# Optimization experiments

Measured on AMD Instinct MI355X. Metric: run time of the kernel, lower is better.

The kernel has to match this reference:

```python
import jax, jax.numpy as jnp
import numpy as np

NUM_HEADS = 8


def setup_inputs() -> dict:
    key = jax.random.key(0)
    k1, k2 = jax.random.split(key)
    B, N_NB, N_C, D = 4, 4, 1024, 512
    d_h = D // NUM_HEADS
    x = jax.random.normal(k1, (B, N_NB, N_C, D), dtype=jnp.float32)
    # GAT-style attention vector a = [a1 || a2], per (batch, neighborhood, head, complex)
    attn_w = jax.random.normal(k2, (B, N_NB, NUM_HEADS, N_C, 2 * d_h), dtype=jnp.float32)
    return {"x": x, "attn_w": attn_w}


def reference(x, attn_w):
    # x: [B, n_neighborhood, n_complexes, D]
    B, N_NB, N_C, D = x.shape
    H = NUM_HEADS
    d_h = D // H
    # split into heads: [B, N_NB, H, N_C, d_h]  (matches reshape + transpose(2,3))
    xh = x.reshape(B, N_NB, N_C, H, d_h).transpose(0, 1, 3, 2, 4)
    # GAT concat-attention: e[b,n,h,i,j] = a1[b,n,h,i] . x_i + a2[b,n,h,i] . x_j
    # (decomposition avoids materializing the [.., N_C, N_C, 2*d_h] concat tensor
    #  that the original builds via repeat / repeat_interleave / cat)
    a1 = attn_w[..., :d_h]   # [B, N_NB, H, N_C, d_h]
    a2 = attn_w[..., d_h:]   # [B, N_NB, H, N_C, d_h]
    e_self = jnp.sum(xh * a1, axis=-1)                    # [B, N_NB, H, N_C]
    e_pair = jnp.einsum('bnhik,bnhjk->bnhij', a2, xh)      # [B, N_NB, H, N_C, N_C]
    scores = e_self[..., None] + e_pair                    # [B, N_NB, H, N_C, N_C]
    attn = jax.nn.softmax(scores, axis=-1)
    # transpose(2,3): heads back next to complexes -> [B, N_NB, N_C, H, N_C]
    return jnp.swapaxes(attn, 2, 3)
```

## Files before the change

### kernel.cpp

```cpp
#include <hip/hip_runtime.h>
#include <hip/hip_fp16.h>


typedef _Float16 half8 __attribute__((ext_vector_type(8)));
typedef float floatx4 __attribute__((ext_vector_type(4)));

#define N_C 1024

__global__ __launch_bounds__(256) void prep_kernel(
    const float* __restrict__ x, _Float16* __restrict__ xh16)
{
  int t = blockIdx.x * 256 + threadIdx.x;
  int kk  = t & 7;
  int row = (t >> 3) & 1023;
  int bnh = t >> 13;
  int bn = bnh >> 3, h = bnh & 7;
  const float* src = x + ((size_t)(bn * N_C + row) * 512) + h * 64 + kk * 8;
  _Float16* dst = xh16 + ((size_t)(bnh * N_C + row) * 64) + ((kk ^ (row & 7)) * 8);
  const float4* s4 = (const float4*)src;
  float4 u = s4[0], v = s4[1];
  half8 hv;
  hv[0] = (_Float16)u.x; hv[1] = (_Float16)u.y;
  hv[2] = (_Float16)u.z; hv[3] = (_Float16)u.w;
  hv[4] = (_Float16)v.x; hv[5] = (_Float16)v.y;
  hv[6] = (_Float16)v.z; hv[7] = (_Float16)v.w;
  *(half8*)dst = hv;
}

__global__ __launch_bounds__(256) void attn_kernel(
    const _Float16* __restrict__ xh16, const float* __restrict__ aw,
    float* __restrict__ out)
{
  __shared__ __align__(16) _Float16 lds[2 * 128 * 64];
  __shared__ float redsum[4][16];

  const int bx  = (blockIdx.x & 7) * 1024 + (blockIdx.x >> 3);
  const int bnh = bx >> 6;
  const int it  = bx & 63;
  const int bn  = bnh >> 3, h = bnh & 7;
  const int tid = threadIdx.x;
  const int w    = tid >> 6;
  const int lane = tid & 63;
  const int l16  = lane & 15;
  const int lq   = lane >> 4;

  const float* a2p = aw + ((size_t)bnh * N_C + it * 16 + l16) * 128 + 64;
  float4 u0 = *(const float4*)(a2p + lq * 8);
  float4 u1 = *(const float4*)(a2p + lq * 8 + 4);
  float4 u2 = *(const float4*)(a2p + 32 + lq * 8);
  float4 u3 = *(const float4*)(a2p + 32 + lq * 8 + 4);
  const float L2E = 1.4426950408889634f;
  half8 afrag0, afrag1;
  afrag0[0] = (_Float16)(u0.x * L2E); afrag0[1] = (_Float16)(u0.y * L2E);
  afrag0[2] = (_Float16)(u0.z * L2E); afrag0[3] = (_Float16)(u0.w * L2E);
  afrag0[4] = (_Float16)(u1.x * L2E); afrag0[5] = (_Float16)(u1.y * L2E);
  afrag0[6] = (_Float16)(u1.z * L2E); afrag0[7] = (_Float16)(u1.w * L2E);
  afrag1[0] = (_Float16)(u2.x * L2E); afrag1[1] = (_Float16)(u2.y * L2E);
  afrag1[2] = (_Float16)(u2.z * L2E); afrag1[3] = (_Float16)(u2.w * L2E);
  afrag1[4] = (_Float16)(u3.x * L2E); afrag1[5] = (_Float16)(u3.y * L2E);
  afrag1[6] = (_Float16)(u3.z * L2E); afrag1[7] = (_Float16)(u3.w * L2E);

  floatx4 acc[16];
  #pragma unroll
  for (int i = 0; i < 16; ++i) acc[i] = floatx4{0.f, 0.f, 0.f, 0.f};
  float rs = 0.f;

  const char* xbase = (const char*)(xh16 + (size_t)bnh * (N_C * 64));
  char* ldsb = (char*)lds;

  #define STAGE(c, b)                                                          \
    _Pragma("unroll")                                                          \
    for (int q = 0; q < 4; ++q) {                                              \
      int seg = (w * 4 + q) * 1024;                                            \
      __builtin_amdgcn_global_load_lds(                                        \
          (const __attribute__((address_space(1))) unsigned int*)              \
              (xbase + (c) * 16384 + seg + lane * 16),                         \
          (__attribute__((address_space(3))) unsigned int*)                    \
              (ldsb + (b) * 16384 + seg),                                      \
          16, 0, 0);                                                           \
    }

  STAGE(0, 0)
  #pragma unroll
  for (int c = 0; c < 8; ++c) {
    const int b = c & 1;
    __syncthreads();
    if (c < 7) STAGE(c + 1, b ^ 1)
    #pragma unroll
    for (int f = 0; f < 2; ++f) {
      int rl = w * 32 + f * 16 + l16;
      const char* p = ldsb + b * 16384 + rl * 128;
      const half8 b0 = *(const half8*)(p + (((lq    ) ^ (rl & 7)) << 4));
      const half8 b1 = *(const half8*)(p + (((lq + 4) ^ (rl & 7)) << 4));
      floatx4 v = acc[c * 2 + f];
      v = __builtin_amdgcn_mfma_f32_16x16x32_f16(b0, afrag0, v, 0, 0, 0);
      v = __builtin_amdgcn_mfma_f32_16x16x32_f16(b1, afrag1, v, 0, 0, 0);
      #pragma unroll
      for (int ri = 0; ri < 4; ++ri) {
        float e = __builtin_amdgcn_exp2f(v[ri]);
        v[ri] = e;
        rs += e;
      }
      acc[c * 2 + f] = v;
    }
  }

  rs += __shfl_xor(rs, 16);
  rs += __shfl_xor(rs, 32);
  if (lane < 16) redsum[w][lane] = rs;
  __syncthreads();
  const float inv = 1.0f / (redsum[0][l16] + redsum[1][l16] +
                            redsum[2][l16] + redsum[3][l16]);

  float* tb = (float*)lds;
  const int W = w * 2048;
  float* orow = out + (((size_t)(bn * N_C + it * 16) * 8 + h) * N_C);
  #pragma unroll
  for (int p = 0; p < 2; ++p) {
    #pragma unroll
    for (int c4 = 0; c4 < 4; ++c4) {
      #pragma unroll
      for (int f = 0; f < 2; ++f) {
        floatx4 v = acc[(p * 4 + c4) * 2 + f] * inv;
        int jl = c4 * 32 + f * 16 + lq * 4;
        *(floatx4*)(tb + W + l16 * 128 + (jl ^ ((l16 & 7) << 2))) = v;
      }
    }
    #pragma unroll
    for (int t = 0; t < 8; ++t) {
      int il = 2 * t + (lane >> 5);
      int jl = (lane & 31) * 4;
      floatx4 v = *(const floatx4*)(tb + W + il * 128 + (jl ^ ((il & 7) << 2)));
      int j = p * 512 + (jl >> 5) * 128 + w * 32 + (jl & 31);
      __builtin_nontemporal_store(v, (floatx4*)(orow + (size_t)il * 8192 + j));
    }
    if (p == 0) __syncthreads();
  }
}

extern "C" void kernel_launch(void* const* d_in, const int* in_sizes, int n_in,
                              void* d_out, int out_size, void* d_ws, size_t ws_size,
                              hipStream_t stream) {
  const float* x  = (const float*)d_in[0];
  const float* aw = (const float*)d_in[1];
  float* out = (float*)d_out;

  _Float16* xh16 = (_Float16*)d_ws;

  prep_kernel<<<4096, 256, 0, stream>>>(x, xh16);
  attn_kernel<<<8192, 256, 0, stream>>>(xh16, aw, out);
}
```

Measured before the change: 125.3 us.

## Fuse fp32-to-fp16 conversion into attention kernel and drop prep kernel

Removes the separate prep kernel that converted x to a swizzled fp16 workspace. Each attention block now loads fp32 x rows directly into registers, converts them to fp16, and writes them into swizzled LDS, with the global load issued before the MFMA work and the LDS write after it so the two overlap. This saves one kernel launch and the workspace write and read-back. The cost is double the L2 read traffic per block (fp32 instead of fp16) and more register pressure from the staging registers. An epilogue __syncthreads is also dropped, since each wave only touches its own LDS region there.

```diff
diff --git a/kernel.cpp b/kernel.cpp
--- a/kernel.cpp
+++ b/kernel.cpp
@@ -7,28 +7,8 @@
 
 #define N_C 1024
 
-__global__ __launch_bounds__(256) void prep_kernel(
-    const float* __restrict__ x, _Float16* __restrict__ xh16)
-{
-  int t = blockIdx.x * 256 + threadIdx.x;
-  int kk  = t & 7;
-  int row = (t >> 3) & 1023;
-  int bnh = t >> 13;
-  int bn = bnh >> 3, h = bnh & 7;
-  const float* src = x + ((size_t)(bn * N_C + row) * 512) + h * 64 + kk * 8;
-  _Float16* dst = xh16 + ((size_t)(bnh * N_C + row) * 64) + ((kk ^ (row & 7)) * 8);
-  const float4* s4 = (const float4*)src;
-  float4 u = s4[0], v = s4[1];
-  half8 hv;
-  hv[0] = (_Float16)u.x; hv[1] = (_Float16)u.y;
-  hv[2] = (_Float16)u.z; hv[3] = (_Float16)u.w;
-  hv[4] = (_Float16)v.x; hv[5] = (_Float16)v.y;
-  hv[6] = (_Float16)v.z; hv[7] = (_Float16)v.w;
-  *(half8*)dst = hv;
-}
-
 __global__ __launch_bounds__(256) void attn_kernel(
-    const _Float16* __restrict__ xh16, const float* __restrict__ aw,
+    const float* __restrict__ x, const float* __restrict__ aw,
     float* __restrict__ out)
 {
   __shared__ __align__(16) _Float16 lds[2 * 128 * 64];
@@ -65,27 +45,38 @@
   for (int i = 0; i < 16; ++i) acc[i] = floatx4{0.f, 0.f, 0.f, 0.f};
   float rs = 0.f;
 
-  const char* xbase = (const char*)(xh16 + (size_t)bnh * (N_C * 64));
-  char* ldsb = (char*)lds;
+  const int sr  = tid >> 1;
+  const int shh = tid & 1;
+  const float* xsrc = x + (((size_t)bn * N_C + sr) * 512) + h * 64 + shh * 32;
+  _Float16* sdst0 = lds + sr * 64;
 
-  #define STAGE(c, b)                                                          \
+  float4 st[8];
+  #define SLOAD(c)                                                             \
     _Pragma("unroll")                                                          \
-    for (int q = 0; q < 4; ++q) {                                              \
-      int seg = (w * 4 + q) * 1024;                                            \
-      __builtin_amdgcn_global_load_lds(                                        \
-          (const __attribute__((address_space(1))) unsigned int*)              \
-              (xbase + (c) * 16384 + seg + lane * 16),                         \
-          (__attribute__((address_space(3))) unsigned int*)                    \
-              (ldsb + (b) * 16384 + seg),                                      \
-          16, 0, 0);                                                           \
+    for (int q = 0; q < 8; ++q)                                                \
+      st[q] = *(const float4*)(xsrc + (size_t)(c) * 65536 + q * 4);
+
+  #define SWRITE(b)                                                            \
+    _Pragma("unroll")                                                          \
+    for (int o = 0; o < 4; ++o) {                                              \
+      half8 hv;                                                                \
+      hv[0] = (_Float16)st[2*o].x;   hv[1] = (_Float16)st[2*o].y;              \
+      hv[2] = (_Float16)st[2*o].z;   hv[3] = (_Float16)st[2*o].w;              \
+      hv[4] = (_Float16)st[2*o+1].x; hv[5] = (_Float16)st[2*o+1].y;            \
+      hv[6] = (_Float16)st[2*o+1].z; hv[7] = (_Float16)st[2*o+1].w;            \
+      int kk = shh * 4 + o;                                                    \
+      *(half8*)(sdst0 + (b) * 8192 + (((kk) ^ (sr & 7)) * 8)) = hv;            \
     }
 
-  STAGE(0, 0)
+  const char* ldsb = (const char*)lds;
+
+  SLOAD(0)
+  SWRITE(0)
   #pragma unroll
   for (int c = 0; c < 8; ++c) {
     const int b = c & 1;
     __syncthreads();
-    if (c < 7) STAGE(c + 1, b ^ 1)
+    if (c < 7) SLOAD(c + 1)
     #pragma unroll
     for (int f = 0; f < 2; ++f) {
       int rl = w * 32 + f * 16 + l16;
@@ -103,6 +94,7 @@
       }
       acc[c * 2 + f] = v;
     }
+    if (c < 7) SWRITE(b ^ 1)
   }
 
   rs += __shfl_xor(rs, 16);
@@ -134,7 +126,6 @@
       int j = p * 512 + (jl >> 5) * 128 + w * 32 + (jl & 31);
       __builtin_nontemporal_store(v, (floatx4*)(orow + (size_t)il * 8192 + j));
     }
-    if (p == 0) __syncthreads();
   }
 }
 
@@ -145,8 +136,5 @@
   const float* aw = (const float*)d_in[1];
   float* out = (float*)d_out;
 
-  _Float16* xh16 = (_Float16*)d_ws;
-
-  prep_kernel<<<4096, 256, 0, stream>>>(x, xh16);
-  attn_kernel<<<8192, 256, 0, stream>>>(xh16, aw, out);
+  attn_kernel<<<8192, 256, 0, stream>>>(x, aw, out);
 }
```

New measurement: 268.1 us. +114.0%, slower.

## Single-buffer LDS staging to raise occupancy, narrow output stores, swizzle prep blocks

Applied to the files above, without the earlier changes.

Halves the attention kernel's LDS by dropping the double buffer, so each chunk is loaded then synced before compute, and adds a launch-bounds hint for 6 blocks per SIMD. The epilogue transpose is reworked into 4 smaller groups with 8-byte nontemporal stores to fit the smaller LDS tile. The prep kernel's block index is also remapped. The intent is more resident blocks to hide the heavily store-bound output traffic, at the cost of losing load/compute overlap and using narrower stores.

```diff
diff --git a/kernel.cpp b/kernel.cpp
--- a/kernel.cpp
+++ b/kernel.cpp
@@ -4,13 +4,15 @@
 
 typedef _Float16 half8 __attribute__((ext_vector_type(8)));
 typedef float floatx4 __attribute__((ext_vector_type(4)));
+typedef float floatx2 __attribute__((ext_vector_type(2)));
 
 #define N_C 1024
 
 __global__ __launch_bounds__(256) void prep_kernel(
     const float* __restrict__ x, _Float16* __restrict__ xh16)
 {
-  int t = blockIdx.x * 256 + threadIdx.x;
+  const int bx = (blockIdx.x & 7) * 512 + (blockIdx.x >> 3);
+  int t = bx * 256 + threadIdx.x;
   int kk  = t & 7;
   int row = (t >> 3) & 1023;
   int bnh = t >> 13;
@@ -27,11 +29,11 @@
   *(half8*)dst = hv;
 }
 
-__global__ __launch_bounds__(256) void attn_kernel(
+__global__ __launch_bounds__(256, 6) void attn_kernel(
     const _Float16* __restrict__ xh16, const float* __restrict__ aw,
     float* __restrict__ out)
 {
-  __shared__ __align__(16) _Float16 lds[2 * 128 * 64];
+  __shared__ __align__(16) _Float16 lds[128 * 64];
   __shared__ float redsum[4][16];
 
   const int bx  = (blockIdx.x & 7) * 1024 + (blockIdx.x >> 3);
@@ -68,28 +70,26 @@
   const char* xbase = (const char*)(xh16 + (size_t)bnh * (N_C * 64));
   char* ldsb = (char*)lds;
 
-  #define STAGE(c, b)                                                          \
+  #define STAGE(c)                                                             \
     _Pragma("unroll")                                                          \
     for (int q = 0; q < 4; ++q) {                                              \
       int seg = (w * 4 + q) * 1024;                                            \
       __builtin_amdgcn_global_load_lds(                                        \
           (const __attribute__((address_space(1))) unsigned int*)              \
               (xbase + (c) * 16384 + seg + lane * 16),                         \
-          (__attribute__((address_space(3))) unsigned int*)                    \
-              (ldsb + (b) * 16384 + seg),                                      \
+          (__attribute__((address_space(3))) unsigned int*)(ldsb + seg),       \
           16, 0, 0);                                                           \
     }
 
-  STAGE(0, 0)
   #pragma unroll
   for (int c = 0; c < 8; ++c) {
-    const int b = c & 1;
     __syncthreads();
-    if (c < 7) STAGE(c + 1, b ^ 1)
+    STAGE(c)
+    __syncthreads();
     #pragma unroll
     for (int f = 0; f < 2; ++f) {
       int rl = w * 32 + f * 16 + l16;
-      const char* p = ldsb + b * 16384 + rl * 128;
+      const char* p = ldsb + rl * 128;
       const half8 b0 = *(const half8*)(p + (((lq    ) ^ (rl & 7)) << 4));
       const half8 b1 = *(const half8*)(p + (((lq + 4) ^ (rl & 7)) << 4));
       floatx4 v = acc[c * 2 + f];
@@ -113,28 +113,27 @@
                             redsum[2][l16] + redsum[3][l16]);
 
   float* tb = (float*)lds;
-  const int W = w * 2048;
+  const int W = w * 1024;
   float* orow = out + (((size_t)(bn * N_C + it * 16) * 8 + h) * N_C);
   #pragma unroll
-  for (int p = 0; p < 2; ++p) {
+  for (int g = 0; g < 4; ++g) {
     #pragma unroll
-    for (int c4 = 0; c4 < 4; ++c4) {
+    for (int cc = 0; cc < 2; ++cc) {
       #pragma unroll
       for (int f = 0; f < 2; ++f) {
-        floatx4 v = acc[(p * 4 + c4) * 2 + f] * inv;
-        int jl = c4 * 32 + f * 16 + lq * 4;
-        *(floatx4*)(tb + W + l16 * 128 + (jl ^ ((l16 & 7) << 2))) = v;
+        floatx4 v = acc[(2 * g + cc) * 2 + f] * inv;
+        int jp = cc * 32 + f * 16 + lq * 4;
+        *(floatx4*)(tb + W + l16 * 64 + (jp ^ ((l16 & 7) << 2))) = v;
       }
     }
     #pragma unroll
     for (int t = 0; t < 8; ++t) {
-      int il = 2 * t + (lane >> 5);
-      int jl = (lane & 31) * 4;
-      floatx4 v = *(const floatx4*)(tb + W + il * 128 + (jl ^ ((il & 7) << 2)));
-      int j = p * 512 + (jl >> 5) * 128 + w * 32 + (jl & 31);
-      __builtin_nontemporal_store(v, (floatx4*)(orow + (size_t)il * 8192 + j));
+      int il  = 2 * t + (lane >> 5);
+      int jp2 = (lane & 31) * 2;
+      floatx2 v = *(const floatx2*)(tb + W + il * 64 + (jp2 ^ ((il & 7) << 2)));
+      int j = g * 256 + (jp2 >> 5) * 128 + w * 32 + (jp2 & 31);
+      __builtin_nontemporal_store(v, (floatx2*)(orow + (size_t)il * 8192 + j));
     }
-    if (p == 0) __syncthreads();
   }
 }
 
```

Result: slower. 132.6 us (+5.9%).
